# Performance work log

Measured on AMD Instinct MI355X. Metric: run time of the kernel, lower is better.

Reference implementation:

```python
import jax, jax.numpy as jnp
import numpy as np

N = 100000
E = 1600000
F_IN = 128
HID = 128
CLS = 40


def setup_inputs() -> dict:
    key = jax.random.key(0)
    ks = jax.random.split(key, 8)
    x = jax.random.normal(ks[0], (N, F_IN), dtype=jnp.float32)
    edge_index = jax.random.randint(ks[1], (2, E), 0, N, dtype=jnp.int64)
    s1 = 1.0 / np.sqrt(F_IN)
    s2 = 1.0 / np.sqrt(HID)
    return {
        "x": x,
        "edge_index": edge_index,
        "Wl1": jax.random.uniform(ks[2], (F_IN, HID), jnp.float32, -s1, s1),
        "Wr1": jax.random.uniform(ks[3], (F_IN, HID), jnp.float32, -s1, s1),
        "b1": jnp.zeros((HID,), jnp.float32),
        "Wl2": jax.random.uniform(ks[4], (HID, CLS), jnp.float32, -s2, s2),
        "Wr2": jax.random.uniform(ks[5], (HID, CLS), jnp.float32, -s2, s2),
        "b2": jnp.zeros((CLS,), jnp.float32),
    }


def _sage_conv(x, src, dst, Wl, Wr, b):
    # mean aggregation of neighbor features: messages flow src -> dst
    msg = x[src]                                                  # [E, F]
    agg = jax.ops.segment_sum(msg, dst, num_segments=N)          # [N, F]
    deg = jax.ops.segment_sum(jnp.ones((src.shape[0],), x.dtype), dst,
                              num_segments=N)                     # [N]
    mean = agg / jnp.maximum(deg, 1.0)[:, None]
    # PyG SAGEConv: lin_l(aggregated) + lin_r(root); bias on lin_l only
    return mean @ Wl + x @ Wr + b


def reference(x, edge_index, Wl1, Wr1, b1, Wl2, Wr2, b2):
    src, dst = edge_index[0], edge_index[1]
    h = _sage_conv(x, src, dst, Wl1, Wr1, b1)
    h = jax.nn.relu(h)
    # dropout is identity in eval mode
    out = _sage_conv(h, src, dst, Wl2, Wr2, b2)
    return out
```

## Files before the change

### kernel.cpp

```cpp
#include <hip/hip_runtime.h>

#define F 128
#define CLSN 40
#define NFINE_MAX 256
#define PCAP 10240
#define TILE 4096
#define STAGE_CAP 10240
#define QSCALE 22.0f

typedef __attribute__((ext_vector_type(8))) short short8v;
typedef __attribute__((ext_vector_type(4))) float float4v;

static __device__ inline ushort f2bf(float f) {
  uint u = __float_as_uint(f);
  uint r = (u + 0x7FFFu + ((u >> 16) & 1u)) >> 16;
  return (ushort)r;
}
static __device__ inline float bfLo(uint u) { return __uint_as_float(u << 16); }
static __device__ inline float bfHi(uint u) { return __uint_as_float(u & 0xFFFF0000u); }
static __device__ inline int sb(uint v, int sh) { return (int)(signed char)(v >> sh); }
static __device__ inline unsigned char q8(float f) {
  float t = rintf(f * QSCALE);
  t = fminf(fmaxf(t, -127.f), 127.f);
  return (unsigned char)(signed char)(int)t;
}
static __device__ inline unsigned char q8s(float f, float qs) {
  float t = rintf(f * qs);
  t = fminf(fmaxf(t, -127.f), 127.f);
  return (unsigned char)(signed char)(int)t;
}

__global__ __launch_bounds__(256) void k_prep(const float* __restrict__ x,
                                              ushort* __restrict__ xb,
                                              unsigned char* __restrict__ xq,
                                              const float* __restrict__ Wl1,
                                              const float* __restrict__ Wr1,
                                              ushort* __restrict__ Wp1,
                                              const float* __restrict__ Wl2,
                                              const float* __restrict__ Wr2,
                                              ushort* __restrict__ Wpl,
                                              ushort* __restrict__ Wpr,
                                              int* __restrict__ fcur,
                                              int nelem4, int castBlocks, int nfine) {
  const int blk = blockIdx.x;
  if (blk < castBlocks) {
    int i = blk * 256 + threadIdx.x;
    if (i < nelem4) {
      float4 v = reinterpret_cast<const float4*>(x)[i];
      ushort4 o;
      o.x = f2bf(v.x); o.y = f2bf(v.y); o.z = f2bf(v.z); o.w = f2bf(v.w);
      reinterpret_cast<ushort4*>(xb)[i] = o;
      uchar4 q;
      q.x = q8(v.x); q.y = q8(v.y); q.z = q8(v.z); q.w = q8(v.w);
      reinterpret_cast<uchar4*>(xq)[i] = q;
    }
  } else if (blk < castBlocks + 16) {
    int t = (blk - castBlocks) * 256 + threadIdx.x;
    int lane = t & 63, f = (t >> 6) & 7, ks = t >> 9;
    int col = f * 16 + (lane & 15);
    int k0 = ks * 32 + (lane >> 4) * 8;
#pragma unroll
    for (int j = 0; j < 8; ++j) {
      int k = k0 + j;
      float w = (k < 128) ? Wl1[k * 128 + col] : Wr1[(k - 128) * 128 + col];
      Wp1[t * 8 + j] = f2bf(w);
    }
  } else if (blk < castBlocks + 22) {
    int t = (blk - castBlocks - 16) * 256 + threadIdx.x;
    const float* W = (t < 768) ? Wl2 : Wr2;
    ushort* Wp = (t < 768) ? Wpl : Wpr;
    int tt = (t < 768) ? t : t - 768;
    int lane = tt & 63, rem = tt >> 6;
    int f = rem % 3, ks = rem / 3;
    int col = f * 16 + (lane & 15);
    int k0 = ks * 32 + (lane >> 4) * 8;
#pragma unroll
    for (int j = 0; j < 8; ++j) {
      int k = k0 + j;
      float w = (col < CLSN) ? W[k * CLSN + col] : 0.f;
      Wp[tt * 8 + j] = f2bf(w);
    }
  } else {
    int i = threadIdx.x;
    if (i < nfine) fcur[i] = i * PCAP;
  }
}

__global__ __launch_bounds__(256) void k_partition(const int* __restrict__ src,
                                                   const int* __restrict__ dst,
                                                   int* __restrict__ fcur,
                                                   uint* __restrict__ pairs, int E) {
  __shared__ int hh[NFINE_MAX];
  __shared__ int bb[NFINE_MAX];
  __shared__ unsigned char ebkt[TILE];
  __shared__ ushort dlow[TILE];
  const int tid = threadIdx.x;
  const int tile0 = blockIdx.x * TILE;
  const int lim = min(TILE, E - tile0);
  for (int i = tid; i < NFINE_MAX; i += 256) hh[i] = 0;
  __syncthreads();
  for (int i = tid; i < lim; i += 256) {
    int d = dst[tile0 + i];
    int b = d >> 9;
    ebkt[i] = (unsigned char)b;
    dlow[i] = (ushort)(d & 511);
    atomicAdd(&hh[b], 1);
  }
  __syncthreads();
  for (int i = tid; i < NFINE_MAX; i += 256) {
    int c = hh[i];
    bb[i] = c ? atomicAdd(&fcur[i], c) : 0;
    hh[i] = 0;
  }
  __syncthreads();
  for (int i = tid; i < lim; i += 256) {
    int b = ebkt[i];
    int r = atomicAdd(&hh[b], 1);
    uint p = (uint)src[tile0 + i] | ((uint)dlow[i] << 17);
    pairs[bb[b] + r] = p;
  }
}

__global__ __launch_bounds__(256) void k_local_scatter(const uint* __restrict__ pairs,
                                                       const int* __restrict__ fcur,
                                                       int* __restrict__ offsets,
                                                       int* __restrict__ srcs,
                                                       int n, int E, int nfine) {
  __shared__ int s_cnt[512];
  __shared__ int s_scan[512];
  __shared__ int s_stage[STAGE_CAP];
  const int b = blockIdx.x, tid = threadIdx.x;
  const int node0 = b << 9;
  const int pbase = b * PCAP;
  int c_i = (tid < nfine) ? (fcur[tid] - tid * PCAP) : 0;
  s_scan[tid] = c_i;
  __syncthreads();
  for (int d = 1; d < 256; d <<= 1) {
    int u = (tid >= d) ? s_scan[tid - d] : 0;
    __syncthreads();
    s_scan[tid] += u;
    __syncthreads();
  }
  const int ecnt = fcur[b] - pbase;
  const int ebase = s_scan[b] - ecnt;
  __syncthreads();
  s_cnt[tid] = 0;
  s_cnt[tid + 256] = 0;
  __syncthreads();
  for (int i = tid; i < ecnt; i += 256) atomicAdd(&s_cnt[pairs[pbase + i] >> 17], 1);
  __syncthreads();
  s_scan[tid] = s_cnt[tid];
  s_scan[tid + 256] = s_cnt[tid + 256];
  __syncthreads();
  for (int d = 1; d < 512; d <<= 1) {
    int v0 = (tid >= d) ? s_scan[tid - d] : 0;
    int v1 = (tid + 256 >= d) ? s_scan[tid + 256 - d] : 0;
    __syncthreads();
    s_scan[tid] += v0;
    s_scan[tid + 256] += v1;
    __syncthreads();
  }
  int e0 = s_scan[tid] - s_cnt[tid];
  int e1 = s_scan[tid + 256] - s_cnt[tid + 256];
  if (node0 + tid < n) offsets[node0 + tid] = ebase + e0;
  if (node0 + tid + 256 < n) offsets[node0 + tid + 256] = ebase + e1;
  if (b == gridDim.x - 1 && tid == 0) offsets[n] = E;
  __syncthreads();
  s_cnt[tid] = e0;
  s_cnt[tid + 256] = e1;
  __syncthreads();
  for (int i = tid; i < ecnt; i += 256) {
    uint p = pairs[pbase + i];
    int v = (int)(p >> 17);
    int s = (int)(p & 0x1FFFFu);
    int pos = atomicAdd(&s_cnt[v], 1);
    if (pos < STAGE_CAP) s_stage[pos] = s;
    else srcs[ebase + pos] = s;
  }
  __syncthreads();
  int lim = min(ecnt, STAGE_CAP);
  for (int i = tid; i < lim; i += 256) srcs[ebase + i] = s_stage[i];
}

__global__ __launch_bounds__(256) void k_agg_x(const unsigned char* __restrict__ xq,
                                               const int* __restrict__ offsets,
                                               const int* __restrict__ srcs,
                                               ushort* __restrict__ mean, int n) {
  const int wid = (blockIdx.x * 256 + threadIdx.x) >> 6;
  const int lane = threadIdx.x & 63;
  const int g = lane >> 4, cl = lane & 15;
  const int node = wid * 4 + g;
  if (node >= n) return;
  const uint2* fp = reinterpret_cast<const uint2*>(xq);
  const int beg = offsets[node];
  const int deg = offsets[node + 1] - beg;
  int s0 = 0, s1 = 0, s2 = 0, s3 = 0, s4 = 0, s5 = 0, s6 = 0, s7 = 0;
  for (int chunk = 0; chunk < deg; chunk += 16) {
    int cnt = min(16, deg - chunk);
    int s = (cl < cnt) ? srcs[beg + chunk + cl] : 0;
    int k = 0;
    for (; k + 7 < cnt; k += 8) {
      int r0 = __shfl(s, g * 16 + k);
      int r1 = __shfl(s, g * 16 + k + 1);
      int r2 = __shfl(s, g * 16 + k + 2);
      int r3 = __shfl(s, g * 16 + k + 3);
      int r4 = __shfl(s, g * 16 + k + 4);
      int r5 = __shfl(s, g * 16 + k + 5);
      int r6 = __shfl(s, g * 16 + k + 6);
      int r7 = __shfl(s, g * 16 + k + 7);
      uint2 v0 = fp[(size_t)r0 * 16 + cl];
      uint2 v1 = fp[(size_t)r1 * 16 + cl];
      uint2 v2 = fp[(size_t)r2 * 16 + cl];
      uint2 v3 = fp[(size_t)r3 * 16 + cl];
      uint2 v4 = fp[(size_t)r4 * 16 + cl];
      uint2 v5 = fp[(size_t)r5 * 16 + cl];
      uint2 v6 = fp[(size_t)r6 * 16 + cl];
      uint2 v7 = fp[(size_t)r7 * 16 + cl];
      s0 += sb(v0.x, 0) + sb(v1.x, 0) + sb(v2.x, 0) + sb(v3.x, 0) +
            sb(v4.x, 0) + sb(v5.x, 0) + sb(v6.x, 0) + sb(v7.x, 0);
      s1 += sb(v0.x, 8) + sb(v1.x, 8) + sb(v2.x, 8) + sb(v3.x, 8) +
            sb(v4.x, 8) + sb(v5.x, 8) + sb(v6.x, 8) + sb(v7.x, 8);
      s2 += sb(v0.x, 16) + sb(v1.x, 16) + sb(v2.x, 16) + sb(v3.x, 16) +
            sb(v4.x, 16) + sb(v5.x, 16) + sb(v6.x, 16) + sb(v7.x, 16);
      s3 += sb(v0.x, 24) + sb(v1.x, 24) + sb(v2.x, 24) + sb(v3.x, 24) +
            sb(v4.x, 24) + sb(v5.x, 24) + sb(v6.x, 24) + sb(v7.x, 24);
      s4 += sb(v0.y, 0) + sb(v1.y, 0) + sb(v2.y, 0) + sb(v3.y, 0) +
            sb(v4.y, 0) + sb(v5.y, 0) + sb(v6.y, 0) + sb(v7.y, 0);
      s5 += sb(v0.y, 8) + sb(v1.y, 8) + sb(v2.y, 8) + sb(v3.y, 8) +
            sb(v4.y, 8) + sb(v5.y, 8) + sb(v6.y, 8) + sb(v7.y, 8);
      s6 += sb(v0.y, 16) + sb(v1.y, 16) + sb(v2.y, 16) + sb(v3.y, 16) +
            sb(v4.y, 16) + sb(v5.y, 16) + sb(v6.y, 16) + sb(v7.y, 16);
      s7 += sb(v0.y, 24) + sb(v1.y, 24) + sb(v2.y, 24) + sb(v3.y, 24) +
            sb(v4.y, 24) + sb(v5.y, 24) + sb(v6.y, 24) + sb(v7.y, 24);
    }
    for (; k < cnt; ++k) {
      int r0 = __shfl(s, g * 16 + k);
      uint2 v0 = fp[(size_t)r0 * 16 + cl];
      s0 += sb(v0.x, 0); s1 += sb(v0.x, 8);
      s2 += sb(v0.x, 16); s3 += sb(v0.x, 24);
      s4 += sb(v0.y, 0); s5 += sb(v0.y, 8);
      s6 += sb(v0.y, 16); s7 += sb(v0.y, 24);
    }
  }
  float inv = deg > 0 ? 1.f / (QSCALE * (float)deg) : 0.f;
  uint4 o;
  o.x = (uint)f2bf((float)s0 * inv) | ((uint)f2bf((float)s1 * inv) << 16);
  o.y = (uint)f2bf((float)s2 * inv) | ((uint)f2bf((float)s3 * inv) << 16);
  o.z = (uint)f2bf((float)s4 * inv) | ((uint)f2bf((float)s5 * inv) << 16);
  o.w = (uint)f2bf((float)s6 * inv) | ((uint)f2bf((float)s7 * inv) << 16);
  reinterpret_cast<uint4*>(mean)[(size_t)node * 16 + cl] = o;
}

__global__ __launch_bounds__(256) void k_mfma1p(const ushort* __restrict__ meanb,
                                                const ushort* __restrict__ rootb,
                                                const ushort* __restrict__ Wp,
                                                const float* __restrict__ b,
                                                const ushort* __restrict__ Wp2l,
                                                const ushort* __restrict__ Wp2r,
                                                const float* __restrict__ b2,
                                                ushort* __restrict__ h,
                                                ushort* __restrict__ p,
                                                float* __restrict__ out,
                                                float* __restrict__ bmax, int nrows) {
  __shared__ __align__(16) ushort As[64 * 256];
  __shared__ float s_wmax[4];
  const int tid = threadIdx.x;
  const int row0 = blockIdx.x * 64;
#pragma unroll
  for (int i = 0; i < 8; ++i) {
    int c = tid + i * 256;
    int r = c >> 5;
    int c16 = c & 31;
    int grow = row0 + r;
    short8v v = {0, 0, 0, 0, 0, 0, 0, 0};
    if (grow < nrows) {
      const ushort* srcp = (c16 < 16) ? (meanb + (size_t)grow * 128 + c16 * 8)
                                      : (rootb + (size_t)grow * 128 + (c16 - 16) * 8);
      v = *reinterpret_cast<const short8v*>(srcp);
    }
    int dbyte = r * 512 + ((c16 * 16) ^ ((r & 7) << 4));
    *reinterpret_cast<short8v*>(reinterpret_cast<char*>(As) + dbyte) = v;
  }
  __syncthreads();
  const int lane = tid & 63;
  const int rbase = (tid >> 6) * 16;
  const int arow = rbase + (lane & 15);
  const int axor = (arow & 7) << 4;
  const short8v* Wp8 = reinterpret_cast<const short8v*>(Wp);
  float4v acc[8];
#pragma unroll
  for (int f = 0; f < 8; ++f) acc[f] = {0.f, 0.f, 0.f, 0.f};
#pragma unroll
  for (int ks = 0; ks < 8; ++ks) {
    int abyte = arow * 512 + ((ks * 64 + (lane >> 4) * 16) ^ axor);
    short8v a = *reinterpret_cast<const short8v*>(reinterpret_cast<const char*>(As) + abyte);
#pragma unroll
    for (int f = 0; f < 8; ++f) {
      short8v bf = Wp8[(ks * 8 + f) * 64 + lane];
      acc[f] = __builtin_amdgcn_mfma_f32_16x16x32_bf16(a, bf, acc[f], 0, 0, 0);
    }
  }
  const int col_lo = lane & 15;
  const int rq = (lane >> 4) * 4;
  __syncthreads();
#pragma unroll
  for (int f = 0; f < 8; ++f) {
    int col = f * 16 + col_lo;
    float bias = b[col];
#pragma unroll
    for (int r = 0; r < 4; ++r) {
      ushort hv = f2bf(fmaxf(acc[f][r] + bias, 0.f));
      int lrow = rbase + rq + r;
      int lbyte = lrow * 256 + (((col >> 3) * 16) ^ ((lrow & 7) << 4)) + (col & 7) * 2;
      *reinterpret_cast<ushort*>(reinterpret_cast<char*>(As) + lbyte) = hv;
    }
  }
  __syncthreads();
#pragma unroll
  for (int i = 0; i < 4; ++i) {
    int c = tid + i * 256;
    int r = c >> 4, c16 = c & 15;
    int grow = row0 + r;
    int lbyte = r * 256 + ((c16 * 16) ^ ((r & 7) << 4));
    short8v v = *reinterpret_cast<const short8v*>(reinterpret_cast<const char*>(As) + lbyte);
    if (grow < nrows)
      *reinterpret_cast<short8v*>(h + (size_t)grow * 128 + c16 * 8) = v;
  }
  const short8v* Wq8 = reinterpret_cast<const short8v*>(Wp2l);
  const short8v* Wr8 = reinterpret_cast<const short8v*>(Wp2r);
  float4v acc2[3], acc3[3];
#pragma unroll
  for (int f = 0; f < 3; ++f) { acc2[f] = {0.f, 0.f, 0.f, 0.f}; acc3[f] = {0.f, 0.f, 0.f, 0.f}; }
#pragma unroll
  for (int ks = 0; ks < 4; ++ks) {
    int abyte = arow * 256 + ((ks * 64 + (lane >> 4) * 16) ^ axor);
    short8v a = *reinterpret_cast<const short8v*>(reinterpret_cast<const char*>(As) + abyte);
#pragma unroll
    for (int f = 0; f < 3; ++f) {
      short8v bfq = Wq8[(ks * 3 + f) * 64 + lane];
      acc2[f] = __builtin_amdgcn_mfma_f32_16x16x32_bf16(a, bfq, acc2[f], 0, 0, 0);
      short8v bfr = Wr8[(ks * 3 + f) * 64 + lane];
      acc3[f] = __builtin_amdgcn_mfma_f32_16x16x32_bf16(a, bfr, acc3[f], 0, 0, 0);
    }
  }
  ushort* Ps = As + 64 * 128;
  float mx = 0.f;
#pragma unroll
  for (int f = 0; f < 3; ++f) {
    int col = f * 16 + col_lo;
#pragma unroll
    for (int r = 0; r < 4; ++r) {
      int lrow = rbase + rq + r;
      int pbyte = lrow * 128 + (((col >> 3) * 16) ^ ((lrow & 7) << 4)) + (col & 7) * 2;
      *reinterpret_cast<ushort*>(reinterpret_cast<char*>(Ps) + pbyte) = f2bf(acc2[f][r]);
      int row = row0 + lrow;
      if (row < nrows) {
        mx = fmaxf(mx, fabsf(acc2[f][r]));
        if (col < CLSN)
          out[(size_t)row * CLSN + col] = acc3[f][r] + b2[col];
      }
    }
  }
#pragma unroll
  for (int r = 0; r < 4; ++r) {
    int lrow = rbase + rq + r;
    int col = 48 + col_lo;
    int pbyte = lrow * 128 + (((col >> 3) * 16) ^ ((lrow & 7) << 4)) + (col & 7) * 2;
    *reinterpret_cast<ushort*>(reinterpret_cast<char*>(Ps) + pbyte) = 0;
  }
  __syncthreads();
#pragma unroll
  for (int i = 0; i < 2; ++i) {
    int c = tid + i * 256;
    int r = c >> 3, c8 = c & 7;
    int grow = row0 + r;
    int lbyte = r * 128 + ((c8 * 16) ^ ((r & 7) << 4));
    short8v v = *reinterpret_cast<const short8v*>(reinterpret_cast<const char*>(Ps) + lbyte);
    if (grow < nrows)
      *reinterpret_cast<short8v*>(p + (size_t)grow * 64 + c8 * 8) = v;
  }
#pragma unroll
  for (int d = 32; d; d >>= 1) mx = fmaxf(mx, __shfl_xor(mx, d));
  if (lane == 0) s_wmax[tid >> 6] = mx;
  __syncthreads();
  if (tid == 0)
    bmax[blockIdx.x] = fmaxf(fmaxf(s_wmax[0], s_wmax[1]), fmaxf(s_wmax[2], s_wmax[3]));
}

__global__ __launch_bounds__(256) void k_scl(const float* __restrict__ bmax,
                                             float* __restrict__ scl, int nb) {
  __shared__ float s_w[4];
  float mx = 0.f;
  for (int i = threadIdx.x; i < nb; i += 256) mx = fmaxf(mx, bmax[i]);
#pragma unroll
  for (int d = 32; d; d >>= 1) mx = fmaxf(mx, __shfl_xor(mx, d));
  if ((threadIdx.x & 63) == 0) s_w[threadIdx.x >> 6] = mx;
  __syncthreads();
  if (threadIdx.x == 0)
    *scl = fmaxf(fmaxf(s_w[0], s_w[1]), fmaxf(s_w[2], s_w[3]));
}

__global__ __launch_bounds__(256) void k_quant_p(const ushort* __restrict__ p,
                                                 const float* __restrict__ scl,
                                                 unsigned char* __restrict__ pq, int nelem4) {
  int i = blockIdx.x * 256 + threadIdx.x;
  if (i >= nelem4) return;
  float ma = *scl;
  float qs = ma > 0.f ? 127.f / ma : 0.f;
  uint2 v = reinterpret_cast<const uint2*>(p)[i];
  uchar4 q;
  q.x = q8s(bfLo(v.x), qs);
  q.y = q8s(bfHi(v.x), qs);
  q.z = q8s(bfLo(v.y), qs);
  q.w = q8s(bfHi(v.y), qs);
  reinterpret_cast<uchar4*>(pq)[i] = q;
}

__global__ __launch_bounds__(256) void k_agg_add(const unsigned char* __restrict__ pq,
                                                 const int* __restrict__ offsets,
                                                 const int* __restrict__ srcs,
                                                 const float* __restrict__ scl,
                                                 float* __restrict__ out, int n) {
  const int wid = (blockIdx.x * 256 + threadIdx.x) >> 6;
  const int lane = threadIdx.x & 63;
  const int g = lane >> 3, cl = lane & 7;
  const int node = wid * 8 + g;
  if (node >= n) return;
  const uint2* pp = reinterpret_cast<const uint2*>(pq);
  const int beg = offsets[node];
  const int deg = offsets[node + 1] - beg;
  int s0 = 0, s1 = 0, s2 = 0, s3 = 0, s4 = 0, s5 = 0, s6 = 0, s7 = 0;
  for (int chunk = 0; chunk < deg; chunk += 8) {
    int cnt = min(8, deg - chunk);
    int s = (cl < cnt) ? srcs[beg + chunk + cl] : 0;
    int k = 0;
    for (; k + 7 < cnt; k += 8) {
      int r0 = __shfl(s, g * 8 + k);
      int r1 = __shfl(s, g * 8 + k + 1);
      int r2 = __shfl(s, g * 8 + k + 2);
      int r3 = __shfl(s, g * 8 + k + 3);
      int r4 = __shfl(s, g * 8 + k + 4);
      int r5 = __shfl(s, g * 8 + k + 5);
      int r6 = __shfl(s, g * 8 + k + 6);
      int r7 = __shfl(s, g * 8 + k + 7);
      uint2 v0 = pp[(size_t)r0 * 8 + cl];
      uint2 v1 = pp[(size_t)r1 * 8 + cl];
      uint2 v2 = pp[(size_t)r2 * 8 + cl];
      uint2 v3 = pp[(size_t)r3 * 8 + cl];
      uint2 v4 = pp[(size_t)r4 * 8 + cl];
      uint2 v5 = pp[(size_t)r5 * 8 + cl];
      uint2 v6 = pp[(size_t)r6 * 8 + cl];
      uint2 v7 = pp[(size_t)r7 * 8 + cl];
      s0 += sb(v0.x, 0) + sb(v1.x, 0) + sb(v2.x, 0) + sb(v3.x, 0) +
            sb(v4.x, 0) + sb(v5.x, 0) + sb(v6.x, 0) + sb(v7.x, 0);
      s1 += sb(v0.x, 8) + sb(v1.x, 8) + sb(v2.x, 8) + sb(v3.x, 8) +
            sb(v4.x, 8) + sb(v5.x, 8) + sb(v6.x, 8) + sb(v7.x, 8);
      s2 += sb(v0.x, 16) + sb(v1.x, 16) + sb(v2.x, 16) + sb(v3.x, 16) +
            sb(v4.x, 16) + sb(v5.x, 16) + sb(v6.x, 16) + sb(v7.x, 16);
      s3 += sb(v0.x, 24) + sb(v1.x, 24) + sb(v2.x, 24) + sb(v3.x, 24) +
            sb(v4.x, 24) + sb(v5.x, 24) + sb(v6.x, 24) + sb(v7.x, 24);
      s4 += sb(v0.y, 0) + sb(v1.y, 0) + sb(v2.y, 0) + sb(v3.y, 0) +
            sb(v4.y, 0) + sb(v5.y, 0) + sb(v6.y, 0) + sb(v7.y, 0);
      s5 += sb(v0.y, 8) + sb(v1.y, 8) + sb(v2.y, 8) + sb(v3.y, 8) +
            sb(v4.y, 8) + sb(v5.y, 8) + sb(v6.y, 8) + sb(v7.y, 8);
      s6 += sb(v0.y, 16) + sb(v1.y, 16) + sb(v2.y, 16) + sb(v3.y, 16) +
            sb(v4.y, 16) + sb(v5.y, 16) + sb(v6.y, 16) + sb(v7.y, 16);
      s7 += sb(v0.y, 24) + sb(v1.y, 24) + sb(v2.y, 24) + sb(v3.y, 24) +
            sb(v4.y, 24) + sb(v5.y, 24) + sb(v6.y, 24) + sb(v7.y, 24);
    }
    for (; k < cnt; ++k) {
      int r0 = __shfl(s, g * 8 + k);
      uint2 v0 = pp[(size_t)r0 * 8 + cl];
      s0 += sb(v0.x, 0); s1 += sb(v0.x, 8);
      s2 += sb(v0.x, 16); s3 += sb(v0.x, 24);
      s4 += sb(v0.y, 0); s5 += sb(v0.y, 8);
      s6 += sb(v0.y, 16); s7 += sb(v0.y, 24);
    }
  }
  if (cl < 5) {
    float ma = *scl;
    float inv = deg > 0 ? ma / (127.f * (float)deg) : 0.f;
    float* op = out + (size_t)node * CLSN + cl * 8;
    float4 a0 = *reinterpret_cast<float4*>(op);
    float4 a1 = *reinterpret_cast<float4*>(op + 4);
    a0.x += (float)s0 * inv; a0.y += (float)s1 * inv;
    a0.z += (float)s2 * inv; a0.w += (float)s3 * inv;
    a1.x += (float)s4 * inv; a1.y += (float)s5 * inv;
    a1.z += (float)s6 * inv; a1.w += (float)s7 * inv;
    *reinterpret_cast<float4*>(op) = a0;
    *reinterpret_cast<float4*>(op + 4) = a1;
  }
}

extern "C" void kernel_launch(void* const* d_in, const int* in_sizes, int n_in,
                              void* d_out, int out_size, void* d_ws, size_t ws_size,
                              hipStream_t stream) {
  const float* x = (const float*)d_in[0];
  const int* ei = (const int*)d_in[1];
  const float* Wl1 = (const float*)d_in[2];
  const float* Wr1 = (const float*)d_in[3];
  const float* b1 = (const float*)d_in[4];
  const float* Wl2 = (const float*)d_in[5];
  const float* Wr2 = (const float*)d_in[6];
  const float* b2 = (const float*)d_in[7];
  float* out = (float*)d_out;

  const int n = in_sizes[0] / F;
  const int E = in_sizes[1] / 2;
  const int* src = ei;
  const int* dst = ei + E;

  const int nfine = (n + 511) >> 9;
  const int ngemm = (n + 63) / 64;

  size_t off = 0;
  auto alloc = [&](size_t bytes) {
    size_t cur = off;
    off = (off + bytes + 255) & ~(size_t)255;
    return cur;
  };
  char* w = (char*)d_ws;
  int* offsets = (int*)(w + alloc((size_t)(n + 1) * 4));
  int* srcs = (int*)(w + alloc((size_t)E * 4));
  int* fcur = (int*)(w + alloc(NFINE_MAX * 4));
  float* scl = (float*)(w + alloc(256));
  float* bmax = (float*)(w + alloc((size_t)(ngemm + 8) * 4));
  ushort* xb = (ushort*)(w + alloc((size_t)n * F * 2));
  ushort* hb = (ushort*)(w + alloc((size_t)n * F * 2));
  ushort* meanb = (ushort*)(w + alloc((size_t)n * F * 2));
  ushort* Wp1 = (ushort*)(w + alloc(32768 * 2));
  ushort* Wp2l = (ushort*)(w + alloc(6144 * 2));
  ushort* Wp2r = (ushort*)(w + alloc(6144 * 2));
  (void)ws_size;
  uint* pairs = (uint*)meanb;
  ushort* p64 = meanb;
  unsigned char* pq8 = (unsigned char*)(meanb + (size_t)n * 64);
  unsigned char* xq8 = (unsigned char*)hb;

  const int castBlocks = (n * 32 + 255) / 256;

  k_prep<<<castBlocks + 23, 256, 0, stream>>>(x, xb, xq8, Wl1, Wr1, Wp1, Wl2, Wr2,
                                              Wp2l, Wp2r, fcur, n * 32, castBlocks,
                                              nfine);

  k_partition<<<(E + TILE - 1) / TILE, 256, 0, stream>>>(src, dst, fcur, pairs, E);
  k_local_scatter<<<nfine, 256, 0, stream>>>(pairs, fcur, offsets, srcs, n, E, nfine);

  k_agg_x<<<(n + 15) / 16, 256, 0, stream>>>(xq8, offsets, srcs, meanb, n);
  k_mfma1p<<<ngemm, 256, 0, stream>>>(meanb, xb, Wp1, b1, Wp2l, Wp2r, b2, hb, p64,
                                      out, bmax, n);

  k_scl<<<1, 256, 0, stream>>>(bmax, scl, ngemm);
  k_quant_p<<<(n * 16 + 255) / 256, 256, 0, stream>>>(p64, scl, pq8, n * 16);
  k_agg_add<<<(n + 31) / 32, 256, 0, stream>>>(pq8, offsets, srcs, scl, out, n);
}
```

Baseline: 174.9 us.

## Fuse edge partition into prep kernel and drop unused hidden-state store

Merges the edge-partitioning pass into the x-cast/weight-pack prep kernel as extra blocks, so partitioning overlaps with the cast instead of running as its own launch. fcur initialisation moves to a tiny separate kernel that runs first. Drops the write of h from the first GEMM kernel, since h is never read again. The p buffer moves into hb so it no longer overlaps meanb. The prep blocks now all reserve the partition's shared memory, which may lower occupancy for the cast blocks.

```diff
diff --git a/kernel.cpp b/kernel.cpp
--- a/kernel.cpp
+++ b/kernel.cpp
@@ -30,21 +30,34 @@
   return (unsigned char)(signed char)(int)t;
 }
 
-__global__ __launch_bounds__(256) void k_prep(const float* __restrict__ x,
-                                              ushort* __restrict__ xb,
-                                              unsigned char* __restrict__ xq,
-                                              const float* __restrict__ Wl1,
-                                              const float* __restrict__ Wr1,
-                                              ushort* __restrict__ Wp1,
-                                              const float* __restrict__ Wl2,
-                                              const float* __restrict__ Wr2,
-                                              ushort* __restrict__ Wpl,
-                                              ushort* __restrict__ Wpr,
-                                              int* __restrict__ fcur,
-                                              int nelem4, int castBlocks, int nfine) {
+__global__ void k_init(int* __restrict__ fcur, int nfine) {
+  int i = threadIdx.x;
+  if (i < nfine) fcur[i] = i * PCAP;
+}
+
+__global__ __launch_bounds__(256) void k_prep2(const float* __restrict__ x,
+                                               ushort* __restrict__ xb,
+                                               unsigned char* __restrict__ xq,
+                                               const float* __restrict__ Wl1,
+                                               const float* __restrict__ Wr1,
+                                               ushort* __restrict__ Wp1,
+                                               const float* __restrict__ Wl2,
+                                               const float* __restrict__ Wr2,
+                                               ushort* __restrict__ Wpl,
+                                               ushort* __restrict__ Wpr,
+                                               const int* __restrict__ srcE,
+                                               const int* __restrict__ dstE,
+                                               int* __restrict__ fcur,
+                                               uint* __restrict__ pairs,
+                                               int nelem4, int castBlocks, int E) {
+  __shared__ int hh[NFINE_MAX];
+  __shared__ int bb[NFINE_MAX];
+  __shared__ unsigned char ebkt[TILE];
+  __shared__ ushort dlow[TILE];
   const int blk = blockIdx.x;
+  const int tid = threadIdx.x;
   if (blk < castBlocks) {
-    int i = blk * 256 + threadIdx.x;
+    int i = blk * 256 + tid;
     if (i < nelem4) {
       float4 v = reinterpret_cast<const float4*>(x)[i];
       ushort4 o;
@@ -55,7 +68,7 @@
       reinterpret_cast<uchar4*>(xq)[i] = q;
     }
   } else if (blk < castBlocks + 16) {
-    int t = (blk - castBlocks) * 256 + threadIdx.x;
+    int t = (blk - castBlocks) * 256 + tid;
     int lane = t & 63, f = (t >> 6) & 7, ks = t >> 9;
     int col = f * 16 + (lane & 15);
     int k0 = ks * 32 + (lane >> 4) * 8;
@@ -66,7 +79,7 @@
       Wp1[t * 8 + j] = f2bf(w);
     }
   } else if (blk < castBlocks + 22) {
-    int t = (blk - castBlocks - 16) * 256 + threadIdx.x;
+    int t = (blk - castBlocks - 16) * 256 + tid;
     const float* W = (t < 768) ? Wl2 : Wr2;
     ushort* Wp = (t < 768) ? Wpl : Wpr;
     int tt = (t < 768) ? t : t - 768;
@@ -81,43 +94,30 @@
       Wp[tt * 8 + j] = f2bf(w);
     }
   } else {
-    int i = threadIdx.x;
-    if (i < nfine) fcur[i] = i * PCAP;
-  }
-}
-
-__global__ __launch_bounds__(256) void k_partition(const int* __restrict__ src,
-                                                   const int* __restrict__ dst,
-                                                   int* __restrict__ fcur,
-                                                   uint* __restrict__ pairs, int E) {
-  __shared__ int hh[NFINE_MAX];
-  __shared__ int bb[NFINE_MAX];
-  __shared__ unsigned char ebkt[TILE];
-  __shared__ ushort dlow[TILE];
-  const int tid = threadIdx.x;
-  const int tile0 = blockIdx.x * TILE;
-  const int lim = min(TILE, E - tile0);
-  for (int i = tid; i < NFINE_MAX; i += 256) hh[i] = 0;
-  __syncthreads();
-  for (int i = tid; i < lim; i += 256) {
-    int d = dst[tile0 + i];
-    int b = d >> 9;
-    ebkt[i] = (unsigned char)b;
-    dlow[i] = (ushort)(d & 511);
-    atomicAdd(&hh[b], 1);
-  }
-  __syncthreads();
-  for (int i = tid; i < NFINE_MAX; i += 256) {
-    int c = hh[i];
-    bb[i] = c ? atomicAdd(&fcur[i], c) : 0;
-    hh[i] = 0;
-  }
-  __syncthreads();
-  for (int i = tid; i < lim; i += 256) {
-    int b = ebkt[i];
-    int r = atomicAdd(&hh[b], 1);
-    uint p = (uint)src[tile0 + i] | ((uint)dlow[i] << 17);
-    pairs[bb[b] + r] = p;
+    const int tile0 = (blk - castBlocks - 22) * TILE;
+    const int lim = min(TILE, E - tile0);
+    for (int i = tid; i < NFINE_MAX; i += 256) hh[i] = 0;
+    __syncthreads();
+    for (int i = tid; i < lim; i += 256) {
+      int d = dstE[tile0 + i];
+      int b = d >> 9;
+      ebkt[i] = (unsigned char)b;
+      dlow[i] = (ushort)(d & 511);
+      atomicAdd(&hh[b], 1);
+    }
+    __syncthreads();
+    for (int i = tid; i < NFINE_MAX; i += 256) {
+      int c = hh[i];
+      bb[i] = c ? atomicAdd(&fcur[i], c) : 0;
+      hh[i] = 0;
+    }
+    __syncthreads();
+    for (int i = tid; i < lim; i += 256) {
+      int b = ebkt[i];
+      int r = atomicAdd(&hh[b], 1);
+      uint p = (uint)srcE[tile0 + i] | ((uint)dlow[i] << 17);
+      pairs[bb[b] + r] = p;
+    }
   }
 }
 
@@ -258,7 +258,6 @@
                                                 const ushort* __restrict__ Wp2l,
                                                 const ushort* __restrict__ Wp2r,
                                                 const float* __restrict__ b2,
-                                                ushort* __restrict__ h,
                                                 ushort* __restrict__ p,
                                                 float* __restrict__ out,
                                                 float* __restrict__ bmax, int nrows) {
@@ -316,16 +315,6 @@
     }
   }
   __syncthreads();
-#pragma unroll
-  for (int i = 0; i < 4; ++i) {
-    int c = tid + i * 256;
-    int r = c >> 4, c16 = c & 15;
-    int grow = row0 + r;
-    int lbyte = r * 256 + ((c16 * 16) ^ ((r & 7) << 4));
-    short8v v = *reinterpret_cast<const short8v*>(reinterpret_cast<const char*>(As) + lbyte);
-    if (grow < nrows)
-      *reinterpret_cast<short8v*>(h + (size_t)grow * 128 + c16 * 8) = v;
-  }
   const short8v* Wq8 = reinterpret_cast<const short8v*>(Wp2l);
   const short8v* Wr8 = reinterpret_cast<const short8v*>(Wp2r);
   float4v acc2[3], acc3[3];
@@ -512,6 +501,7 @@
 
   const int nfine = (n + 511) >> 9;
   const int ngemm = (n + 63) / 64;
+  const int partBlocks = (E + TILE - 1) / TILE;
 
   size_t off = 0;
   auto alloc = [&](size_t bytes) {
@@ -533,21 +523,21 @@
   ushort* Wp2r = (ushort*)(w + alloc(6144 * 2));
   (void)ws_size;
   uint* pairs = (uint*)meanb;
-  ushort* p64 = meanb;
+  unsigned char* xq8 = (unsigned char*)hb;
+  ushort* p64 = hb + (size_t)n * 64;
   unsigned char* pq8 = (unsigned char*)(meanb + (size_t)n * 64);
-  unsigned char* xq8 = (unsigned char*)hb;
 
   const int castBlocks = (n * 32 + 255) / 256;
 
-  k_prep<<<castBlocks + 23, 256, 0, stream>>>(x, xb, xq8, Wl1, Wr1, Wp1, Wl2, Wr2,
-                                              Wp2l, Wp2r, fcur, n * 32, castBlocks,
-                                              nfine);
-
-  k_partition<<<(E + TILE - 1) / TILE, 256, 0, stream>>>(src, dst, fcur, pairs, E);
+  k_init<<<1, 256, 0, stream>>>(fcur, nfine);
+  k_prep2<<<castBlocks + 22 + partBlocks, 256, 0, stream>>>(
+      x, xb, xq8, Wl1, Wr1, Wp1, Wl2, Wr2, Wp2l, Wp2r, src, dst, fcur, pairs,
+      n * 32, castBlocks, E);
+
   k_local_scatter<<<nfine, 256, 0, stream>>>(pairs, fcur, offsets, srcs, n, E, nfine);
 
   k_agg_x<<<(n + 15) / 16, 256, 0, stream>>>(xq8, offsets, srcs, meanb, n);
-  k_mfma1p<<<ngemm, 256, 0, stream>>>(meanb, xb, Wp1, b1, Wp2l, Wp2r, b2, hb, p64,
+  k_mfma1p<<<ngemm, 256, 0, stream>>>(meanb, xb, Wp1, b1, Wp2l, Wp2r, b2, p64,
                                       out, bmax, n);
 
   k_scl<<<1, 256, 0, stream>>>(bmax, scl, ngemm);
```

After: 186.4 us. 1.07x slower.
